# Kernel tuning notes

Hardware: AMD Instinct MI355X
Metric: run time of the kernel (lower is better)

## Reference

```python
import jax, jax.numpy as jnp
import numpy as np
from jax import lax

NUM_HEADS = 4
ROPE_BASE = 10000.0


def _rope(x):
    # x: (b, h, w, c). Faithful to the torch RoPE: angles indexed by the h axis
    # with shape (h, c/2), which broadcasts against the w axis (requires h == w).
    b, h, w, c = x.shape
    k_max = c // 2
    theta = 1.0 / (ROPE_BASE ** (jnp.arange(k_max, dtype=x.dtype) / k_max))  # (c/2,)
    angles = jnp.arange(h, dtype=x.dtype)[:, None] * theta  # (h, c/2)
    cos, sin = jnp.cos(angles), jnp.sin(angles)
    xr = x.reshape(b, h, w, k_max, 2)
    re, im = xr[..., 0], xr[..., 1]
    # complex multiply (cos + i sin) * (re + i im); (h, c/2) broadcasts along w
    out_re = cos * re - sin * im
    out_im = sin * re + cos * im
    return jnp.stack([out_re, out_im], axis=-1).reshape(b, h, w, c)


def setup_inputs() -> dict:
    key = jax.random.key(0)
    k1, k2, k3, k4, k5 = jax.random.split(key, 5)
    b, c, h, w = 8, 512, 96, 96
    x = jax.random.normal(k1, (b, c, h, w), dtype=jnp.float32)
    W_qk = jax.random.normal(k2, (2 * c, c), dtype=jnp.float32) * (c ** -0.5)
    b_qk = jax.random.normal(k3, (2 * c,), dtype=jnp.float32) * 0.02
    lepe_w = jax.random.normal(k4, (c, 1, 3, 3), dtype=jnp.float32) * (1.0 / 3.0)
    lepe_b = jax.random.normal(k5, (c,), dtype=jnp.float32) * 0.02
    return {"x": x, "W_qk": W_qk, "b_qk": b_qk, "lepe_w": lepe_w, "lepe_b": lepe_b}


def reference(x, W_qk, b_qk, lepe_w, lepe_b):
    b, c, h, w = x.shape
    n = h * w
    heads = NUM_HEADS
    hd = c // heads

    xs = x.reshape(b, c, n).transpose(0, 2, 1)  # (b, n, c)
    qk = (xs @ W_qk.T + b_qk).reshape(b, n, 2, c)
    q = jax.nn.elu(qk[:, :, 0]) + 1.0  # (b, n, c)
    k = jax.nn.elu(qk[:, :, 1]) + 1.0
    v = xs

    q_rope = _rope(q.reshape(b, h, w, c)).reshape(b, n, heads, hd).transpose(0, 2, 1, 3)
    k_rope = _rope(k.reshape(b, h, w, c)).reshape(b, n, heads, hd).transpose(0, 2, 1, 3)

    # faithful flat reshape (b, n, c) -> (b, heads, n, hd) (splits the n axis)
    q2 = q.reshape(b, heads, n, hd)
    k2 = k.reshape(b, heads, n, hd)
    v2 = v.reshape(b, heads, n, hd)

    k_mean = k2.mean(axis=2, keepdims=True)  # (b, heads, 1, hd)
    z = 1.0 / (jnp.einsum('bhnd,bhmd->bhnm', q2, k_mean) + 1e-6)  # (b, heads, n, 1)

    scale = n ** -0.5
    kv = jnp.einsum('bhnd,bhne->bhde', k_rope * scale, v2 * scale)  # (b, heads, hd, hd)
    out = jnp.einsum('bhnd,bhde->bhne', q_rope, kv) * z  # (b, heads, n, hd)

    out = out.transpose(0, 2, 1, 3).reshape(b, n, c).transpose(0, 2, 1).reshape(b, c, h, w)

    # v2.reshape(b,h,w,c).permute(0,3,1,2) recovers the original (b, c, h, w) layout
    v_img = v2.reshape(b, h, w, c).transpose(0, 3, 1, 2)
    lepe = lax.conv_general_dilated(
        v_img, lepe_w, window_strides=(1, 1), padding='SAME',
        feature_group_count=c, dimension_numbers=('NCHW', 'OIHW', 'NCHW'))
    lepe = lepe + lepe_b[None, :, None, None]
    return out + lepe
```

## Files before the change

kernel.cpp:

```cpp
#include <hip/hip_runtime.h>
#include <hip/hip_bf16.h>
#include <cstdint>

#define BB 8
#define CC 512
#define HH 96
#define NN 9216
#define HEADS 4
#define HD 128
#define KMAX 256

typedef unsigned short ushort_t;
typedef __attribute__((ext_vector_type(8))) short bf16x8;
typedef __attribute__((ext_vector_type(4))) float f32x4;

__device__ __forceinline__ unsigned short f2bf(float f) {
  unsigned int u = __float_as_uint(f);
  u += 0x7fffu + ((u >> 16) & 1u);
  return (unsigned short)(u >> 16);
}
__device__ __forceinline__ float bf2f(unsigned short s) {
  return __uint_as_float(((unsigned int)s) << 16);
}
__device__ __forceinline__ unsigned int pk2(float lo, float hi) {
  return (unsigned int)f2bf(lo) | ((unsigned int)f2bf(hi) << 16);
}

__device__ __forceinline__ void gld16(const void* g, void* l) {
  __builtin_amdgcn_global_load_lds(
      (const __attribute__((address_space(1))) unsigned int*)(uintptr_t)g,
      (__attribute__((address_space(3))) unsigned int*)(unsigned int)(uintptr_t)l,
      16, 0, 0);
}

__global__ void rope_table_k(float* __restrict__ rope) {
  int t = blockIdx.x * 256 + threadIdx.x;
  if (t >= HH * KMAX) return;
  int col = t >> 8;
  int kk = t & (KMAX - 1);
  float theta = powf(10000.0f, -((float)kk) / (float)KMAX);
  float ang = (float)col * theta;
  float s, c;
  sincosf(ang, &s, &c);
  rope[2 * t] = c;
  rope[2 * t + 1] = s;
}

__global__ void conv_w_k(const float* __restrict__ W, unsigned short* __restrict__ Wbf) {
  int t = blockIdx.x * 256 + threadIdx.x;
  float4 v = *(const float4*)(W + (size_t)t * 4);
  unsigned int lo = (unsigned int)f2bf(v.x) | ((unsigned int)f2bf(v.y) << 16);
  unsigned int hi = (unsigned int)f2bf(v.z) | ((unsigned int)f2bf(v.w) << 16);
  *(uint2*)(Wbf + (size_t)t * 4) = make_uint2(lo, hi);
}

__global__ void transpose_all_k(const float* __restrict__ x, unsigned short* __restrict__ xt) {
  __shared__ unsigned short T[64 * 72];
  const int pos0 = blockIdx.x * 64;
  const int ch0 = blockIdx.y * 64;
  const int b = blockIdx.z;
  const int tid = threadIdx.x;
#pragma unroll
  for (int i = 0; i < 4; ++i) {
    int fi = i * 256 + tid;
    int ch = fi >> 4, p4 = fi & 15;
    float4 v = *(const float4*)(x + ((size_t)b * CC + ch0 + ch) * NN + pos0 + p4 * 4);
    T[(p4 * 4 + 0) * 72 + ch] = f2bf(v.x);
    T[(p4 * 4 + 1) * 72 + ch] = f2bf(v.y);
    T[(p4 * 4 + 2) * 72 + ch] = f2bf(v.z);
    T[(p4 * 4 + 3) * 72 + ch] = f2bf(v.w);
  }
  __syncthreads();
#pragma unroll
  for (int i = 0; i < 2; ++i) {
    int s = i * 256 + tid;
    int p = s >> 3, cc = s & 7;
    uint4 u = *(const uint4*)&T[p * 72 + cc * 8];
    *(uint4*)(xt + ((size_t)b * NN + pos0 + p) * CC + ch0 + cc * 8) = u;
  }
}

__launch_bounds__(256)
__global__ void gemm_qk_mfma(const unsigned short* __restrict__ xtall,
                             const unsigned short* __restrict__ Wbf,
                             const float* __restrict__ bqk,
                             unsigned short* __restrict__ qout,
                             unsigned short* __restrict__ kout,
                             float* __restrict__ ksum) {
  __shared__ __align__(16) unsigned short sA[128 * 64];
  __shared__ __align__(16) unsigned short sB[128 * 64];
  const int flat = blockIdx.x;
  const int bn = (flat >> 3) & 7;
  const int g = ((flat >> 6) << 3) | (flat & 7);
  const int b = g / 72;
  const int m0 = (g - b * 72) * 128;
  const int tid = threadIdx.x;
  const int wv = tid >> 6, lane = tid & 63;
  const int j0 = bn * 128;
  const unsigned short* xt = xtall + (size_t)b * NN * CC;
  const int row = lane & 15, quad = lane >> 4;
  const int jt0 = (wv & 1) * 64, pt0 = (wv >> 1) * 64;
  f32x4 acc[4][4];
#pragma unroll
  for (int ji = 0; ji < 4; ++ji)
#pragma unroll
    for (int pi = 0; pi < 4; ++pi) acc[ji][pi] = (f32x4){0.f, 0.f, 0.f, 0.f};

  for (int kt = 0; kt < CC; kt += 64) {
#pragma unroll
    for (int it = 0; it < 4; ++it) {
      int s = it * 256 + tid;
      int srow = s >> 3;
      int sc = (s & 7) ^ (srow & 7);
      int ldsoff = (it * 256 + wv * 64) * 8;
      gld16(xt + (size_t)(m0 + srow) * CC + kt + sc * 8, &sA[ldsoff]);
      gld16(Wbf + (size_t)(j0 + srow) * CC + kt + sc * 8, &sB[ldsoff]);
    }
    __syncthreads();
#pragma unroll
    for (int ks = 0; ks < 2; ++ks) {
      bf16x8 aw[4], ax[4];
      const int chunk = (ks * 4 + quad) ^ (row & 7);
#pragma unroll
      for (int ji = 0; ji < 4; ++ji)
        aw[ji] = *(const bf16x8*)&sB[((jt0 + ji * 16 + row) * 8 + chunk) * 8];
#pragma unroll
      for (int pi = 0; pi < 4; ++pi)
        ax[pi] = *(const bf16x8*)&sA[((pt0 + pi * 16 + row) * 8 + chunk) * 8];
#pragma unroll
      for (int ji = 0; ji < 4; ++ji)
#pragma unroll
        for (int pi = 0; pi < 4; ++pi)
          acc[ji][pi] = __builtin_amdgcn_mfma_f32_16x16x32_bf16(aw[ji], ax[pi], acc[ji][pi], 0, 0, 0);
    }
    __syncthreads();
  }
  unsigned short* dst = (j0 < CC) ? qout : kout;
  const int jl0 = j0 & (CC - 1);
  const int pq = (m0 >> 7) / 18;
#pragma unroll
  for (int ji = 0; ji < 4; ++ji) {
    const float4 bb = *(const float4*)&bqk[j0 + jt0 + ji * 16 + quad * 4];
    const float bj[4] = {bb.x, bb.y, bb.z, bb.w};
    float sacc[4] = {0.f, 0.f, 0.f, 0.f};
#pragma unroll
    for (int pi = 0; pi < 4; ++pi) {
      float v[4];
#pragma unroll
      for (int r = 0; r < 4; ++r) {
        float t = acc[ji][pi][r] + bj[r];
        v[r] = t > 0.f ? t + 1.f : __expf(t);
        sacc[r] += v[r];
      }
      const int posm = m0 + pt0 + pi * 16 + row;
      uint2 pkd = make_uint2(pk2(v[0], v[1]), pk2(v[2], v[3]));
      *(uint2*)&dst[((size_t)b * NN + posm) * CC + jl0 + jt0 + ji * 16 + quad * 4] = pkd;
    }
    if (j0 >= CC) {
#pragma unroll
      for (int r = 0; r < 4; ++r) {
        float s = sacc[r];
        s += __shfl_xor(s, 1);
        s += __shfl_xor(s, 2);
        s += __shfl_xor(s, 4);
        s += __shfl_xor(s, 8);
        if (row == 0)
          atomicAdd(&ksum[((size_t)b * 4 + pq) * 512 + jl0 + jt0 + ji * 16 + quad * 4 + r], s);
      }
    }
  }
}

__global__ void z_k(const unsigned short* __restrict__ qbf, const float* __restrict__ ksum,
                    float* __restrict__ z) {
  const int wv = threadIdx.x >> 6, lane = threadIdx.x & 63;
  const int zbase = (blockIdx.x * 4 + wv) * 8;
  const int bh = zbase / NN;
  const int p0 = zbase % NN;
  const int b = bh >> 2, head = bh & 3;
  const float* ks = ksum + (size_t)bh * 512;
  const int d0 = lane * 2;
  const float km0 = (ks[d0] + ks[d0 + 128] + ks[d0 + 256] + ks[d0 + 384]) * (1.0f / 9216.0f);
  const float km1 = (ks[d0 + 1] + ks[d0 + 129] + ks[d0 + 257] + ks[d0 + 385]) * (1.0f / 9216.0f);
#pragma unroll
  for (int it = 0; it < 8; ++it) {
    const int p = p0 + it;
    const int pos = head * 2304 + (p >> 2);
    const int chb = (p & 3) * 128;
    const unsigned short* qp = qbf + ((size_t)b * NN + pos) * CC + chb + lane * 2;
    float dot = bf2f(qp[0]) * km0 + bf2f(qp[1]) * km1;
#pragma unroll
    for (int off = 1; off < 64; off <<= 1) dot += __shfl_xor(dot, off, 64);
    if (lane == 0) z[zbase + it] = 1.0f / (dot + 1e-6f);
  }
}

__launch_bounds__(256, 2)
__global__ void kv_mfma_k(const unsigned short* __restrict__ kbf, const float* __restrict__ x,
                          const float* __restrict__ rope, float* __restrict__ kvp) {
  __shared__ __align__(16) unsigned short sK[128 * 64];
  const int s = blockIdx.x;
  const int bh = blockIdx.y;
  const int b = bh >> 2, head = bh & 3;
  const int tid = threadIdx.x;
  const int wv = tid >> 6, lane = tid & 63;
  const int row = lane & 15, quad = lane >> 4;
  const int e0 = (wv & 1) * 64, d0 = (wv >> 1) * 64;
  const int r = s >> 2;
  const int t0 = (s & 3) * 576;

  const int qg = tid & 7;
  const int dg = (tid >> 3) * 4;
  const unsigned short* kbase = kbf + (size_t)b * NN * CC + head * HD + dg;
  const int pairb = head * 64 + (dg >> 1);

  f32x4 acc[4][4];
#pragma unroll
  for (int mi = 0; mi < 4; ++mi)
#pragma unroll
    for (int ni = 0; ni < 4; ++ni) acc[mi][ni] = (f32x4){0.f, 0.f, 0.f, 0.f};

  for (int ck = 0; ck < 9; ++ck) {
    const int tc = t0 + ck * 64;
    float4 a0[8], a1[8];
#pragma unroll
    for (int mi = 0; mi < 4; ++mi)
#pragma unroll
      for (int ks = 0; ks < 2; ++ks) {
        const float* xp = x + (size_t)(b * CC + r * 128 + e0 + mi * 16 + row) * NN +
                          head * 2304 + tc + ks * 32 + quad * 8;
        a0[mi * 2 + ks] = *(const float4*)xp;
        a1[mi * 2 + ks] = *(const float4*)(xp + 4);
      }
    {
      int p = 4 * (tc + qg * 8) + r;
      int col = p % 96;
      float rw0[8], rw1[8], rw2[8], rw3[8];
#pragma unroll
      for (int j = 0; j < 8; ++j) {
        uint2 kv2 = *(const uint2*)(kbase + (size_t)p * CC);
        const float* rp = rope + ((size_t)col * KMAX + pairb) * 2;
        float4 cs = *(const float4*)rp;
        float re0 = bf2f((unsigned short)(kv2.x & 0xffffu));
        float im0 = bf2f((unsigned short)(kv2.x >> 16));
        float re1 = bf2f((unsigned short)(kv2.y & 0xffffu));
        float im1 = bf2f((unsigned short)(kv2.y >> 16));
        rw0[j] = cs.x * re0 - cs.y * im0;
        rw1[j] = cs.y * re0 + cs.x * im0;
        rw2[j] = cs.z * re1 - cs.w * im1;
        rw3[j] = cs.w * re1 + cs.z * im1;
        p += 4;
        col += 4;
        col = (col >= 96) ? col - 96 : col;
      }
#pragma unroll
      for (int rr = 0; rr < 4; ++rr) {
        const float* rw = (rr == 0) ? rw0 : (rr == 1) ? rw1 : (rr == 2) ? rw2 : rw3;
        const int d = dg + rr;
        uint4 pk;
        pk.x = pk2(rw[0], rw[1]);
        pk.y = pk2(rw[2], rw[3]);
        pk.z = pk2(rw[4], rw[5]);
        pk.w = pk2(rw[6], rw[7]);
        *(uint4*)&sK[(d * 8 + (qg ^ (d & 7))) * 8] = pk;
      }
    }
    __syncthreads();
#pragma unroll
    for (int ks = 0; ks < 2; ++ks) {
      bf16x8 bfr[4];
#pragma unroll
      for (int ni = 0; ni < 4; ++ni) {
        const int d = d0 + ni * 16 + row;
        const int o = (ks * 4 + quad) ^ (d & 7);
        bfr[ni] = *(const bf16x8*)&sK[(d * 8 + o) * 8];
      }
#pragma unroll
      for (int mi = 0; mi < 4; ++mi) {
        const int f = mi * 2 + ks;
        union { bf16x8 v; unsigned int u[4]; } af;
        af.u[0] = pk2(a0[f].x, a0[f].y);
        af.u[1] = pk2(a0[f].z, a0[f].w);
        af.u[2] = pk2(a1[f].x, a1[f].y);
        af.u[3] = pk2(a1[f].z, a1[f].w);
#pragma unroll
        for (int ni = 0; ni < 4; ++ni)
          acc[mi][ni] = __builtin_amdgcn_mfma_f32_16x16x32_bf16(af.v, bfr[ni], acc[mi][ni], 0, 0, 0);
      }
    }
    __syncthreads();
  }
  float* dst = kvp + (size_t)(s * 32 + bh) * (HD * HD);
#pragma unroll
  for (int mi = 0; mi < 4; ++mi) {
#pragma unroll
    for (int ni = 0; ni < 4; ++ni) {
#pragma unroll
      for (int rr = 0; rr < 4; ++rr) {
        const int e = e0 + mi * 16 + quad * 4 + rr;
        const int d = d0 + ni * 16 + row;
        dst[e * HD + d] = acc[mi][ni][rr];
      }
    }
  }
}

__global__ void kv_reduce_k(const float* __restrict__ kvp, unsigned short* __restrict__ kvtb) {
  int idx = blockIdx.x * 256 + threadIdx.x;
  float ssum = 0.f;
#pragma unroll
  for (int i = 0; i < 16; ++i) ssum += kvp[(size_t)i * (32 * HD * HD) + idx];
  kvtb[idx] = f2bf(ssum * (1.0f / 9216.0f));
}

__launch_bounds__(256)
__global__ void out_mfma_k(const unsigned short* __restrict__ qbf,
                           const unsigned short* __restrict__ kvtb,
                           const float* __restrict__ z, const float* __restrict__ rope,
                           float* __restrict__ out) {
  __shared__ __align__(16) float Ts[64 * 132];
  unsigned short* sQ = (unsigned short*)Ts;
  const int bh = blockIdx.y, b = bh >> 2, head = bh & 3;
  const int pos0 = blockIdx.x * 128;
  const int tid = threadIdx.x, wv = tid >> 6, lane = tid & 63;
  const int row = lane & 15, quad = lane >> 4;
  const int e0 = (wv & 1) * 64;
  const int p0 = (wv >> 1) * 64;

#pragma unroll
  for (int it = 0; it < 8; ++it) {
    const int s = it * 256 + tid;
    const int srow = s >> 4, sc = s & 15;
    const int scs = (sc & 8) | ((sc & 7) ^ (srow & 7));
    gld16(qbf + ((size_t)b * NN + pos0 + srow) * CC + head * HD + scs * 8,
          &sQ[(size_t)(it * 256 + wv * 64) * 8]);
  }

  f32x4 acc[4][4];
#pragma unroll
  for (int mi = 0; mi < 4; ++mi)
#pragma unroll
    for (int ni = 0; ni < 4; ++ni) acc[mi][ni] = (f32x4){0.f, 0.f, 0.f, 0.f};

  int posn[4], coln[4];
#pragma unroll
  for (int ni = 0; ni < 4; ++ni) {
    posn[ni] = pos0 + p0 + ni * 16 + row;
    coln[ni] = posn[ni] % 96;
  }
  __syncthreads();

#pragma unroll
  for (int kt = 0; kt < HD; kt += 32) {
    bf16x8 af[4], bfr[4];
#pragma unroll
    for (int mi = 0; mi < 4; ++mi)
      af[mi] = *(const bf16x8*)&kvtb[((size_t)bh * HD + e0 + mi * 16 + row) * HD + kt + quad * 8];
#pragma unroll
    for (int ni = 0; ni < 4; ++ni) {
      const int posL = p0 + ni * 16 + row;
      const int chb = (kt >> 3) + quad;
      const int cl = (chb & 8) | ((chb & 7) ^ (posL & 7));
      const uint4 u = *(const uint4*)&sQ[posL * 128 + cl * 8];
      const int pairb = head * 64 + (kt >> 1) + quad * 4;
      const float* rp = rope + ((size_t)coln[ni] * KMAX + pairb) * 2;
      float4 r0 = *(const float4*)rp;
      float4 r1 = *(const float4*)(rp + 4);
      unsigned int uu[4] = {u.x, u.y, u.z, u.w};
      float cs[8] = {r0.x, r0.y, r0.z, r0.w, r1.x, r1.y, r1.z, r1.w};
      bf16x8 bb;
#pragma unroll
      for (int pr = 0; pr < 4; ++pr) {
        float re = bf2f((unsigned short)(uu[pr] & 0xffffu));
        float im = bf2f((unsigned short)(uu[pr] >> 16));
        float c = cs[2 * pr], s = cs[2 * pr + 1];
        bb[2 * pr] = (short)f2bf(c * re - s * im);
        bb[2 * pr + 1] = (short)f2bf(s * re + c * im);
      }
      bfr[ni] = bb;
    }
#pragma unroll
    for (int mi = 0; mi < 4; ++mi)
#pragma unroll
      for (int ni = 0; ni < 4; ++ni)
        acc[mi][ni] = __builtin_amdgcn_mfma_f32_16x16x32_bf16(af[mi], bfr[ni], acc[mi][ni], 0, 0, 0);
  }
#pragma unroll
  for (int ni = 0; ni < 4; ++ni) {
    const float zn = z[(size_t)bh * NN + posn[ni]];
#pragma unroll
    for (int mi = 0; mi < 4; ++mi)
#pragma unroll
      for (int r = 0; r < 4; ++r) acc[mi][ni][r] *= zn;
  }
  __syncthreads();

#pragma unroll
  for (int h = 0; h < 2; ++h) {
    if ((wv & 1) == h) {
#pragma unroll
      for (int mi = 0; mi < 4; ++mi)
#pragma unroll
        for (int ni = 0; ni < 4; ++ni)
#pragma unroll
          for (int r = 0; r < 4; ++r) {
            const int eL = mi * 16 + quad * 4 + r;
            const int p = p0 + ni * 16 + row;
            Ts[eL * 132 + p] = acc[mi][ni][r];
          }
    }
    __syncthreads();
#pragma unroll
    for (int i = 0; i < 8; ++i) {
      const int eL = i * 8 + (tid >> 5);
      const int c = tid & 31;
      const float4 vv = *(const float4*)&Ts[eL * 132 + c * 4];
      *(float4*)&out[((size_t)b * CC + head * HD + h * 64 + eL) * NN + pos0 + c * 4] = vv;
    }
    __syncthreads();
  }
}

__global__ void lepe_k(const float* __restrict__ x, const float* __restrict__ lw,
                       const float* __restrict__ lb, float* __restrict__ out) {
  const int blk = blockIdx.x;
  const int bc = blk / 9;
  const int tile = blk - bc * 9;
  const int ch = bc & (CC - 1);
  const float* wp = lw + ch * 9;
  float w[9];
#pragma unroll
  for (int t = 0; t < 9; ++t) w[t] = wp[t];
  const float bias = lb[ch];
  const float* xp = x + (size_t)bc * NN;
  const int pos = tile * 1024 + threadIdx.x * 4;
  const int pi = pos / 96;
  const int pj = pos - pi * 96;

  float4 o = *(const float4*)(out + (size_t)bc * NN + pos);

  float a0 = bias, a1 = bias, a2 = bias, a3 = bias;
#pragma unroll
  for (int r = 0; r < 3; ++r) {
    const int y = pi + r - 1;
    if ((unsigned)y >= 96u) continue;
    const float* rowp = xp + y * 96 + pj;
    float4 M = *(const float4*)rowp;
    float Lv = (pj > 0) ? rowp[-1] : 0.f;
    float Rv = (pj < 92) ? rowp[4] : 0.f;
    const float w0 = w[r * 3 + 0], w1 = w[r * 3 + 1], w2 = w[r * 3 + 2];
    a0 += w0 * Lv + w1 * M.x + w2 * M.y;
    a1 += w0 * M.x + w1 * M.y + w2 * M.z;
    a2 += w0 * M.y + w1 * M.z + w2 * M.w;
    a3 += w0 * M.z + w1 * M.w + w2 * Rv;
  }
  o.x += a0; o.y += a1; o.z += a2; o.w += a3;
  *(float4*)(out + (size_t)bc * NN + pos) = o;
}

extern "C" void kernel_launch(void* const* d_in, const int* in_sizes, int n_in,
                              void* d_out, int out_size, void* d_ws, size_t ws_size,
                              hipStream_t stream) {
  const float* x = (const float*)d_in[0];
  const float* Wqk = (const float*)d_in[1];
  const float* bqk = (const float*)d_in[2];
  const float* lw = (const float*)d_in[3];
  const float* lb = (const float*)d_in[4];
  float* out = (float*)d_out;
  char* ws = (char*)d_ws;
  unsigned short* qbf = (unsigned short*)(ws);
  unsigned short* kbf = (unsigned short*)(ws + 75497472);
  float* rope = (float*)(ws + 150994944);
  float* z = (float*)(ws + 151207936);
  float* kvp = (float*)(ws + 152387584);
  float* ksum = (float*)(ws + 152387584);
  unsigned short* kvtb = (unsigned short*)(ws + 185942016);
  unsigned short* Wbf = (unsigned short*)(ws + 188039168);
  unsigned short* xtb = (unsigned short*)d_out;

  hipMemsetAsync(ksum, 0, (size_t)BB * 4 * 512 * sizeof(float), stream);
  conv_w_k<<<dim3(512), dim3(256), 0, stream>>>(Wqk, Wbf);
  rope_table_k<<<dim3(96), dim3(256), 0, stream>>>(rope);
  transpose_all_k<<<dim3(144, 8, 8), dim3(256), 0, stream>>>(x, xtb);
  gemm_qk_mfma<<<dim3(4608), dim3(256), 0, stream>>>(xtb, Wbf, bqk, qbf, kbf, ksum);
  z_k<<<dim3(9216), dim3(256), 0, stream>>>(qbf, ksum, z);
  kv_mfma_k<<<dim3(16, 32), dim3(256), 0, stream>>>(kbf, x, rope, kvp);
  kv_reduce_k<<<dim3(2048), dim3(256), 0, stream>>>(kvp, kvtb);
  out_mfma_k<<<dim3(72, 32), dim3(256), 0, stream>>>(qbf, kvtb, z, rope, out);
  lepe_k<<<dim3(36864), dim3(256), 0, stream>>>(x, lw, lb, out);
}
```

Before: 713.2 us.

## Double-buffer QK GEMM LDS loads and replace atomic ksum with partial-sum reduction

The QK projection GEMM now uses two LDS buffers, prefetching the next K-tile with async global-to-LDS loads while MFMAs run on the current one, synchronised by explicit vmcnt waits and barriers. The k-sum atomics are replaced by deterministic per-block partial writes, and a new small kmean kernel reduces them before z_k, which also removes the memset. The cost is doubled LDS per block, which may lower occupancy, plus one extra launch.

```diff
diff --git a/kernel.cpp b/kernel.cpp
--- a/kernel.cpp
+++ b/kernel.cpp
@@ -86,14 +86,15 @@
                              const float* __restrict__ bqk,
                              unsigned short* __restrict__ qout,
                              unsigned short* __restrict__ kout,
-                             float* __restrict__ ksum) {
-  __shared__ __align__(16) unsigned short sA[128 * 64];
-  __shared__ __align__(16) unsigned short sB[128 * 64];
+                             float* __restrict__ kpart) {
+  __shared__ __align__(16) unsigned short sA[2 * 128 * 64];
+  __shared__ __align__(16) unsigned short sB[2 * 128 * 64];
   const int flat = blockIdx.x;
   const int bn = (flat >> 3) & 7;
   const int g = ((flat >> 6) << 3) | (flat & 7);
   const int b = g / 72;
-  const int m0 = (g - b * 72) * 128;
+  const int mblk = g - b * 72;
+  const int m0 = mblk * 128;
   const int tid = threadIdx.x;
   const int wv = tid >> 6, lane = tid & 63;
   const int j0 = bn * 128;
@@ -106,38 +107,49 @@
 #pragma unroll
     for (int pi = 0; pi < 4; ++pi) acc[ji][pi] = (f32x4){0.f, 0.f, 0.f, 0.f};
 
-  for (int kt = 0; kt < CC; kt += 64) {
+  auto STAGE = [&](int kt, int buf) {
 #pragma unroll
     for (int it = 0; it < 4; ++it) {
       int s = it * 256 + tid;
       int srow = s >> 3;
       int sc = (s & 7) ^ (srow & 7);
-      int ldsoff = (it * 256 + wv * 64) * 8;
+      int ldsoff = buf * 8192 + (it * 256 + wv * 64) * 8;
       gld16(xt + (size_t)(m0 + srow) * CC + kt + sc * 8, &sA[ldsoff]);
       gld16(Wbf + (size_t)(j0 + srow) * CC + kt + sc * 8, &sB[ldsoff]);
     }
-    __syncthreads();
+  };
+
+  STAGE(0, 0);
+  for (int ktI = 0; ktI < 8; ++ktI) {
+    const int cur = ktI & 1;
+    if (ktI < 7) {
+      STAGE((ktI + 1) * 64, cur ^ 1);
+      asm volatile("s_waitcnt vmcnt(8)" ::: "memory");
+    } else {
+      asm volatile("s_waitcnt vmcnt(0)" ::: "memory");
+    }
+    __builtin_amdgcn_sched_barrier(0);
+    __builtin_amdgcn_s_barrier();
 #pragma unroll
     for (int ks = 0; ks < 2; ++ks) {
       bf16x8 aw[4], ax[4];
       const int chunk = (ks * 4 + quad) ^ (row & 7);
 #pragma unroll
       for (int ji = 0; ji < 4; ++ji)
-        aw[ji] = *(const bf16x8*)&sB[((jt0 + ji * 16 + row) * 8 + chunk) * 8];
+        aw[ji] = *(const bf16x8*)&sB[cur * 8192 + ((jt0 + ji * 16 + row) * 8 + chunk) * 8];
 #pragma unroll
       for (int pi = 0; pi < 4; ++pi)
-        ax[pi] = *(const bf16x8*)&sA[((pt0 + pi * 16 + row) * 8 + chunk) * 8];
+        ax[pi] = *(const bf16x8*)&sA[cur * 8192 + ((pt0 + pi * 16 + row) * 8 + chunk) * 8];
 #pragma unroll
       for (int ji = 0; ji < 4; ++ji)
 #pragma unroll
         for (int pi = 0; pi < 4; ++pi)
           acc[ji][pi] = __builtin_amdgcn_mfma_f32_16x16x32_bf16(aw[ji], ax[pi], acc[ji][pi], 0, 0, 0);
     }
-    __syncthreads();
+    __builtin_amdgcn_s_barrier();
   }
   unsigned short* dst = (j0 < CC) ? qout : kout;
   const int jl0 = j0 & (CC - 1);
-  const int pq = (m0 >> 7) / 18;
 #pragma unroll
   for (int ji = 0; ji < 4; ++ji) {
     const float4 bb = *(const float4*)&bqk[j0 + jt0 + ji * 16 + quad * 4];
@@ -165,23 +177,34 @@
         s += __shfl_xor(s, 4);
         s += __shfl_xor(s, 8);
         if (row == 0)
-          atomicAdd(&ksum[((size_t)b * 4 + pq) * 512 + jl0 + jt0 + ji * 16 + quad * 4 + r], s);
-      }
-    }
-  }
-}
-
-__global__ void z_k(const unsigned short* __restrict__ qbf, const float* __restrict__ ksum,
+          kpart[((size_t)(b * 72 + mblk) * 2 + (pt0 >> 6)) * 512 +
+                jl0 + jt0 + ji * 16 + quad * 4 + r] = s;
+      }
+    }
+  }
+}
+
+__global__ void kmean_k(const float* __restrict__ kpart, float* __restrict__ kmean) {
+  int idx = blockIdx.x * 256 + threadIdx.x;
+  int bh = idx >> 7, d = idx & 127;
+  int b = bh >> 2, head = bh & 3;
+  float s = 0.f;
+  for (int i = 0; i < 36; ++i) {
+    const float* p = kpart + ((size_t)(b * 72 + head * 18) * 2 + i) * 512 + d;
+    s += p[0] + p[128] + p[256] + p[384];
+  }
+  kmean[idx] = s * (1.0f / 9216.0f);
+}
+
+__global__ void z_k(const unsigned short* __restrict__ qbf, const float* __restrict__ kmean,
                     float* __restrict__ z) {
   const int wv = threadIdx.x >> 6, lane = threadIdx.x & 63;
   const int zbase = (blockIdx.x * 4 + wv) * 8;
   const int bh = zbase / NN;
   const int p0 = zbase % NN;
   const int b = bh >> 2, head = bh & 3;
-  const float* ks = ksum + (size_t)bh * 512;
-  const int d0 = lane * 2;
-  const float km0 = (ks[d0] + ks[d0 + 128] + ks[d0 + 256] + ks[d0 + 384]) * (1.0f / 9216.0f);
-  const float km1 = (ks[d0 + 1] + ks[d0 + 129] + ks[d0 + 257] + ks[d0 + 385]) * (1.0f / 9216.0f);
+  const float km0 = kmean[bh * 128 + lane * 2];
+  const float km1 = kmean[bh * 128 + lane * 2 + 1];
 #pragma unroll
   for (int it = 0; it < 8; ++it) {
     const int p = p0 + it;
@@ -473,17 +496,18 @@
   float* rope = (float*)(ws + 150994944);
   float* z = (float*)(ws + 151207936);
   float* kvp = (float*)(ws + 152387584);
-  float* ksum = (float*)(ws + 152387584);
+  float* kpart = (float*)(ws + 152387584);
+  float* kmean = (float*)(ws + 152387584 + 1179648);
   unsigned short* kvtb = (unsigned short*)(ws + 185942016);
   unsigned short* Wbf = (unsigned short*)(ws + 188039168);
   unsigned short* xtb = (unsigned short*)d_out;
 
-  hipMemsetAsync(ksum, 0, (size_t)BB * 4 * 512 * sizeof(float), stream);
   conv_w_k<<<dim3(512), dim3(256), 0, stream>>>(Wqk, Wbf);
   rope_table_k<<<dim3(96), dim3(256), 0, stream>>>(rope);
   transpose_all_k<<<dim3(144, 8, 8), dim3(256), 0, stream>>>(x, xtb);
-  gemm_qk_mfma<<<dim3(4608), dim3(256), 0, stream>>>(xtb, Wbf, bqk, qbf, kbf, ksum);
-  z_k<<<dim3(9216), dim3(256), 0, stream>>>(qbf, ksum, z);
+  gemm_qk_mfma<<<dim3(4608), dim3(256), 0, stream>>>(xtb, Wbf, bqk, qbf, kbf, kpart);
+  kmean_k<<<dim3(16), dim3(256), 0, stream>>>(kpart, kmean);
+  z_k<<<dim3(9216), dim3(256), 0, stream>>>(qbf, kmean, z);
   kv_mfma_k<<<dim3(16, 32), dim3(256), 0, stream>>>(kbf, x, rope, kvp);
   kv_reduce_k<<<dim3(2048), dim3(256), 0, stream>>>(kvp, kvtb);
   out_mfma_k<<<dim3(72, 32), dim3(256), 0, stream>>>(qbf, kvtb, z, rope, out);
```

Result: faster. 698.2 us (-2.1%).
